# Optimization experiments

Hardware: AMD Instinct MI355X
Metric: run time of the kernel (lower is better)

## Reference

```python
import jax, jax.numpy as jnp
import numpy as np

B, S, D = 2, 2048, 2048
NH, NKV, HD = 32, 8, 64
ROPE_BASE = 10000.0


def rope(x):
    # x: [b, s, h, d]; torchtune-style interleaved-pair RoPE
    b, s, h, d = x.shape
    pos = jnp.arange(s, dtype=jnp.float32)
    inv_freq = 1.0 / (ROPE_BASE ** (jnp.arange(0, d, 2, dtype=jnp.float32) / d))
    ang = pos[:, None] * inv_freq[None, :]            # [s, d//2]
    cos = jnp.cos(ang)[None, :, None, :].astype(x.dtype)
    sin = jnp.sin(ang)[None, :, None, :].astype(x.dtype)
    xr = x.reshape(b, s, h, d // 2, 2)
    x0, x1 = xr[..., 0], xr[..., 1]
    out = jnp.stack([x0 * cos - x1 * sin, x0 * sin + x1 * cos], axis=-1)
    return out.reshape(b, s, h, d)


def setup_inputs() -> dict:
    key = jax.random.key(0)
    ks = jax.random.split(key, 5)
    return {
        "x": jax.random.normal(ks[0], (B, S, D), dtype=jnp.float32),
        "Wq": jax.random.normal(ks[1], (NH * HD, D), dtype=jnp.float32) * 0.02,
        "Wk": jax.random.normal(ks[2], (NKV * HD, D), dtype=jnp.float32) * 0.02,
        "Wv": jax.random.normal(ks[3], (NKV * HD, D), dtype=jnp.float32) * 0.02,
        "Wo": jax.random.normal(ks[4], (D, NH * HD), dtype=jnp.float32) * 0.02,
    }


def reference(x, Wq, Wk, Wv, Wo):
    b, s, _ = x.shape
    qpk = NH // NKV  # queries per kv head
    # projections (Linear, no bias)
    q = (x @ Wq.T).reshape(b, s, NH, HD)
    k = (x @ Wk.T).reshape(b, s, NKV, HD)
    v = (x @ Wv.T).reshape(b, s, NKV, HD)
    # RoPE on q and k (expanding k before RoPE == RoPE on kv heads then group-broadcast)
    q = rope(q)
    k = rope(k)
    # grouped attention: q -> [b, s, g, n, d], k/v stay [b, s, g, d]
    qg = q.reshape(b, s, NKV, qpk, HD)
    scale = 1.0 / jnp.sqrt(jnp.array(HD, dtype=x.dtype))
    scores = jnp.einsum("bqgnd,bkgd->bgnqk", qg, k) * scale  # [b,g,n,s,s]
    attn = jax.nn.softmax(scores, axis=-1)
    out = jnp.einsum("bgnqk,bkgd->bqgnd", attn, v)           # [b,s,g,n,d]
    out = out.reshape(b, s, NH * HD)
    return out @ Wo.T
```

## Files before the change

### kernel.cpp

```cpp
#include <hip/hip_runtime.h>
#include <hip/hip_bf16.h>
#include <math.h>

#define SLEN 2048
#define DMODEL 2048
#define NH 32
#define NKV 8
#define HD 64
#define BATCH 2
#define MROWS (BATCH * SLEN)
#define QKVN (NH * HD + 2 * NKV * HD)

typedef __attribute__((ext_vector_type(8))) short bf16x8;
typedef __attribute__((ext_vector_type(4))) float f32x4;
typedef __attribute__((ext_vector_type(16))) float f32x16;
typedef __attribute__((ext_vector_type(4))) unsigned u32x4;

__device__ __forceinline__ unsigned short f2bf(float f) {
  union { float f; unsigned u; } v; v.f = f;
  return (unsigned short)((v.u + 0x7FFFu + ((v.u >> 16) & 1u)) >> 16);
}
__device__ __forceinline__ float bf2f(unsigned short h) {
  union { unsigned u; float f; } v; v.u = ((unsigned)h) << 16;
  return v.f;
}
__device__ __forceinline__ unsigned cvt_pk_bf16(float lo, float hi) {
  unsigned r;
  asm("v_cvt_pk_bf16_f32 %0, %1, %2" : "=v"(r) : "v"(lo), "v"(hi));
  return r;
}
__device__ __forceinline__ float fast_exp2(float x) {
#if __has_builtin(__builtin_amdgcn_exp2f)
  return __builtin_amdgcn_exp2f(x);
#else
  return exp2f(x);
#endif
}
__device__ __forceinline__ void gload_lds16(const unsigned short* g, unsigned short* l) {
  __builtin_amdgcn_global_load_lds(
      (const __attribute__((address_space(1))) unsigned int*)(g),
      (__attribute__((address_space(3))) unsigned int*)(l), 16, 0, 0);
}

__global__ __launch_bounds__(256) void cvt_kernel(const float* __restrict__ src,
                                                  unsigned short* __restrict__ dst,
                                                  int n8) {
  const int i = blockIdx.x * 256 + threadIdx.x;
  if (i >= n8) return;
  const float4 a = *(const float4*)&src[(size_t)i * 8];
  const float4 b = *(const float4*)&src[(size_t)i * 8 + 4];
  uint4 o;
  o.x = cvt_pk_bf16(a.x, a.y);
  o.y = cvt_pk_bf16(a.z, a.w);
  o.z = cvt_pk_bf16(b.x, b.y);
  o.w = cvt_pk_bf16(b.z, b.w);
  *(uint4*)&dst[(size_t)i * 8] = o;
}

__global__ __launch_bounds__(256) void cvt_w4_kernel(
    const float* __restrict__ Wq, const float* __restrict__ Wk,
    const float* __restrict__ Wv, const float* __restrict__ Wo,
    unsigned short* __restrict__ wqkvb, unsigned short* __restrict__ wob) {
  const int i = blockIdx.x * 256 + threadIdx.x;
  const float* src;
  unsigned short* dst;
  size_t off;
  if (i < 524288)       { src = Wq; dst = wqkvb;           off = i; }
  else if (i < 655360)  { src = Wk; dst = wqkvb + 4194304; off = i - 524288; }
  else if (i < 786432)  { src = Wv; dst = wqkvb + 5242880; off = i - 655360; }
  else                  { src = Wo; dst = wob;             off = i - 786432; }
  const float4 a = *(const float4*)&src[off * 8];
  const float4 b = *(const float4*)&src[off * 8 + 4];
  uint4 o;
  o.x = cvt_pk_bf16(a.x, a.y);
  o.y = cvt_pk_bf16(a.z, a.w);
  o.z = cvt_pk_bf16(b.x, b.y);
  o.w = cvt_pk_bf16(b.z, b.w);
  *(uint4*)&dst[off * 8] = o;
}

template <int OUTBF16>
__global__ __launch_bounds__(256) void gemm_bf16_kernel(
    const unsigned short* __restrict__ A, const unsigned short* __restrict__ B,
    void* __restrict__ Cv, int M, int N, int K) {
  __shared__ unsigned short As[128][32];
  __shared__ unsigned short Bs[128][32];

  const int tid = threadIdx.x;
  const int lane = tid & 63;
  const int wid = tid >> 6;
  const int g = lane >> 4;
  const int fr = lane & 15;
  const int m0 = blockIdx.x * 128;
  const int n0 = blockIdx.y * 128;
  const int wm = (wid >> 1) * 64;
  const int wn = (wid & 1) * 64;

  const int srow = wid * 32 + (lane >> 2);
  const int scol = (lane & 3) * 8;
  const unsigned short* ga = &A[(size_t)(m0 + srow) * K + scol];
  const unsigned short* gb = &B[(size_t)(n0 + srow) * K + scol];
  unsigned short* la0 = &As[wid * 32][0];
  unsigned short* la1 = &As[wid * 32 + 16][0];
  unsigned short* lb0 = &Bs[wid * 32][0];
  unsigned short* lb1 = &Bs[wid * 32 + 16][0];
  const size_t rstep = (size_t)16 * K;

  f32x4 acc[4][4];
#pragma unroll
  for (int i = 0; i < 4; i++)
#pragma unroll
    for (int j = 0; j < 4; j++) acc[i][j] = (f32x4){0.f, 0.f, 0.f, 0.f};

  for (int kt = 0; kt < K; kt += 32) {
    __syncthreads();
    gload_lds16(ga + kt, la0);
    gload_lds16(ga + kt + rstep, la1);
    gload_lds16(gb + kt, lb0);
    gload_lds16(gb + kt + rstep, lb1);
    __syncthreads();

    bf16x8 af[4], bfr[4];
#pragma unroll
    for (int i = 0; i < 4; i++) {
      af[i] = *(const bf16x8*)&As[wm + i * 16 + fr][g * 8];
      bfr[i] = *(const bf16x8*)&Bs[wn + i * 16 + fr][g * 8];
    }
#pragma unroll
    for (int i = 0; i < 4; i++)
#pragma unroll
      for (int j = 0; j < 4; j++)
        acc[i][j] = __builtin_amdgcn_mfma_f32_16x16x32_bf16(af[i], bfr[j], acc[i][j], 0, 0, 0);
  }

  if constexpr (OUTBF16) {
    unsigned short* C = (unsigned short*)Cv;
#pragma unroll
    for (int i = 0; i < 4; i++)
#pragma unroll
      for (int j = 0; j < 4; j++)
#pragma unroll
        for (int r = 0; r < 4; r++)
          C[(size_t)(m0 + wm + i * 16 + g * 4 + r) * N + n0 + wn + j * 16 + fr] =
              f2bf(acc[i][j][r]);
  } else {
    float* C = (float*)Cv;
#pragma unroll
    for (int i = 0; i < 4; i++)
#pragma unroll
      for (int j = 0; j < 4; j++)
#pragma unroll
        for (int r = 0; r < 4; r++)
          C[(size_t)(m0 + wm + i * 16 + g * 4 + r) * N + n0 + wn + j * 16 + fr] =
              acc[i][j][r];
  }
}

__global__ __launch_bounds__(256) void rope_q_kernel(const unsigned short* __restrict__ qkvb,
                                                     unsigned short* __restrict__ qb) {
  const int idx = blockIdx.x * 256 + threadIdx.x;
  const int j = idx & 31;
  const int s = (idx >> 5) & (SLEN - 1);
  const int h = (idx >> 16) & (NH - 1);
  const int b = idx >> 21;
  const unsigned pin = *(const unsigned*)&qkvb[(size_t)(b * SLEN + s) * QKVN + h * HD + 2 * j];
  const float x0 = bf2f((unsigned short)(pin & 0xffffu));
  const float x1 = bf2f((unsigned short)(pin >> 16));
  const float inv = expf(-0.14391156831f * (float)(2 * j));
  const float ang = (float)s * inv;
  float sn, cs;
  sincosf(ang, &sn, &cs);
  const float SC = 0.18033688011f;
  const float o0 = (x0 * cs - x1 * sn) * SC;
  const float o1 = (x0 * sn + x1 * cs) * SC;
  *(unsigned*)&qb[((size_t)(b * NH + h) * SLEN + s) * HD + 2 * j] = cvt_pk_bf16(o0, o1);
}

__global__ __launch_bounds__(256) void rope_k_kernel(const unsigned short* __restrict__ qkvb,
                                                     unsigned short* __restrict__ kb) {
  const int idx = blockIdx.x * 256 + threadIdx.x;
  const int j = idx & 31;
  const int s = (idx >> 5) & (SLEN - 1);
  const int kh = (idx >> 16) & (NKV - 1);
  const int b = idx >> 19;
  const unsigned pin =
      *(const unsigned*)&qkvb[(size_t)(b * SLEN + s) * QKVN + NH * HD + kh * HD + 2 * j];
  const float x0 = bf2f((unsigned short)(pin & 0xffffu));
  const float x1 = bf2f((unsigned short)(pin >> 16));
  const float inv = expf(-0.14391156831f * (float)(2 * j));
  const float ang = (float)s * inv;
  float sn, cs;
  sincosf(ang, &sn, &cs);
  const float o0 = x0 * cs - x1 * sn;
  const float o1 = x0 * sn + x1 * cs;
  *(unsigned*)&kb[((size_t)(b * NKV + kh) * SLEN + s) * HD + 2 * j] = cvt_pk_bf16(o0, o1);
}

__global__ __launch_bounds__(256) void vcast_kernel(const unsigned short* __restrict__ qkvb,
                                                    unsigned short* __restrict__ vt) {
  __shared__ unsigned short tile[64][72];
  const int tid = threadIdx.x;
  const int bi = blockIdx.x;
  const int st = bi & 31;
  const int kh = (bi >> 5) & 7;
  const int b = bi >> 8;
  const int r = tid >> 2;
  const int c0 = (tid & 3) * 16;
  const unsigned short* src =
      &qkvb[(size_t)(b * SLEN + st * 64 + r) * QKVN + (NH + NKV) * HD + kh * HD + c0];
  *(bf16x8*)&tile[r][c0] = *(const bf16x8*)src;
  *(bf16x8*)&tile[r][c0 + 8] = *(const bf16x8*)(src + 8);
  __syncthreads();
  alignas(16) unsigned short tmp[16];
#pragma unroll
  for (int i = 0; i < 16; ++i) tmp[i] = tile[c0 + i][r];
  unsigned short* dst = &vt[((size_t)(b * NKV + kh) * HD + r) * SLEN + st * 64 + c0];
  *(bf16x8*)dst = *(bf16x8*)tmp;
  *(bf16x8*)(dst + 8) = *(bf16x8*)(tmp + 8);
}

__global__ __launch_bounds__(512) void attn_kernel(
    const unsigned short* __restrict__ qb, const unsigned short* __restrict__ kb,
    const unsigned short* __restrict__ vt, unsigned short* __restrict__ aob) {
  __shared__ unsigned short Kbuf[2][4096];
  __shared__ unsigned short Vbuf[2][4096];

  const int tid = threadIdx.x;
  const int lane = tid & 63;
  const int wid = tid >> 6;
  const int lq = lane & 31;
  const int hi = lane >> 5;
  const int sw = lane & 7;

  const int jb = blockIdx.x;
  const int xcd = jb & 7;
  const int idx = jb >> 3;
  const int bh = xcd * 8 + (idx & 7);
  const int qt = idx >> 3;
  const int b = bh >> 5, h = bh & 31;
  const int kh = h >> 2;
  const size_t qbase = (size_t)bh * SLEN * HD;
  const size_t kbase = (size_t)(b * NKV + kh) * SLEN * HD;
  const size_t vbase = (size_t)(b * NKV + kh) * HD * SLEN;

  const int q0 = qt * 256 + wid * 32;
  bf16x8 qf[4];
#pragma unroll
  for (int ks = 0; ks < 4; ++ks)
    qf[ks] = *(const bf16x8*)&qb[qbase + (size_t)(q0 + lq) * HD + ks * 16 + hi * 8];

  const int swzc = ((lane & 7) ^ ((lane >> 3) & 7)) * 8;
  const int srow = wid * 8 + (lane >> 3);
  const unsigned short* gk0 = kb + kbase + (size_t)srow * HD + swzc;
  const unsigned short* gv0 = vt + vbase + (size_t)srow * SLEN + swzc;

  f32x16 acc0 = {}, acc1 = {};
  float m = -1e30f, l = 0.f;

  gload_lds16(gk0, &Kbuf[0][wid * 512]);
  gload_lds16(gv0, &Vbuf[0][wid * 512]);

  for (int kt = 0; kt < SLEN / 64; ++kt) {
    const int cur = kt & 1;
    asm volatile("s_waitcnt vmcnt(0)" ::: "memory");
    __syncthreads();
    if (kt + 1 < SLEN / 64) {
      const int nxt = cur ^ 1;
      const size_t ko = (size_t)(kt + 1) * 64 * HD;
      const size_t vo = (size_t)(kt + 1) * 64;
      gload_lds16(gk0 + ko, &Kbuf[nxt][wid * 512]);
      gload_lds16(gv0 + vo, &Vbuf[nxt][wid * 512]);
    }

    f32x16 s0 = {}, s1 = {};
#pragma unroll
    for (int ks = 0; ks < 4; ++ks) {
      const bf16x8 kf = *(const bf16x8*)&Kbuf[cur][lq * HD + (((ks * 2 + hi) ^ sw) * 8)];
      s0 = __builtin_amdgcn_mfma_f32_32x32x16_bf16(kf, qf[ks], s0, 0, 0, 0);
    }
#pragma unroll
    for (int ks = 0; ks < 4; ++ks) {
      const bf16x8 kf = *(const bf16x8*)&Kbuf[cur][(32 + lq) * HD + (((ks * 2 + hi) ^ sw) * 8)];
      s1 = __builtin_amdgcn_mfma_f32_32x32x16_bf16(kf, qf[ks], s1, 0, 0, 0);
    }

    float tm = s0[0];
#pragma unroll
    for (int i = 1; i < 16; ++i) tm = fmaxf(tm, s0[i]);
#pragma unroll
    for (int i = 0; i < 16; ++i) tm = fmaxf(tm, s1[i]);
    tm = fmaxf(tm, __shfl_xor(tm, 32));

    if (__any(tm > m + 8.0f)) {
      const float mn = fmaxf(m, tm);
      const float corr = fast_exp2(m - mn);
      l *= corr;
#pragma unroll
      for (int i = 0; i < 16; ++i) { acc0[i] *= corr; acc1[i] *= corr; }
      m = mn;
    }

    float p0[16], p1[16];
    float lsum = 0.f;
#pragma unroll
    for (int i = 0; i < 16; ++i) { p0[i] = fast_exp2(s0[i] - m); lsum += p0[i]; }
#pragma unroll
    for (int i = 0; i < 16; ++i) { p1[i] = fast_exp2(s1[i] - m); lsum += p1[i]; }
    lsum += __shfl_xor(lsum, 32);
    l += lsum;

    unsigned u0[8], u1[8];
#pragma unroll
    for (int c = 0; c < 4; ++c) {
      u0[2 * c] = cvt_pk_bf16(p0[4 * c], p0[4 * c + 1]);
      u0[2 * c + 1] = cvt_pk_bf16(p0[4 * c + 2], p0[4 * c + 3]);
      u1[2 * c] = cvt_pk_bf16(p1[4 * c], p1[4 * c + 1]);
      u1[2 * c + 1] = cvt_pk_bf16(p1[4 * c + 2], p1[4 * c + 3]);
    }
    bf16x8 pf[4];
    {
      unsigned a0 = u0[0], b0 = u0[2];
      asm volatile("v_permlane32_swap_b32 %0, %1" : "+v"(a0), "+v"(b0));
      unsigned a1 = u0[1], b1 = u0[3];
      asm volatile("v_permlane32_swap_b32 %0, %1" : "+v"(a1), "+v"(b1));
      u32x4 t = {a0, a1, b0, b1};
      pf[0] = __builtin_bit_cast(bf16x8, t);
      unsigned a2 = u0[4], b2 = u0[6];
      asm volatile("v_permlane32_swap_b32 %0, %1" : "+v"(a2), "+v"(b2));
      unsigned a3 = u0[5], b3 = u0[7];
      asm volatile("v_permlane32_swap_b32 %0, %1" : "+v"(a3), "+v"(b3));
      u32x4 t2 = {a2, a3, b2, b3};
      pf[1] = __builtin_bit_cast(bf16x8, t2);
      unsigned a4 = u1[0], b4 = u1[2];
      asm volatile("v_permlane32_swap_b32 %0, %1" : "+v"(a4), "+v"(b4));
      unsigned a5 = u1[1], b5 = u1[3];
      asm volatile("v_permlane32_swap_b32 %0, %1" : "+v"(a5), "+v"(b5));
      u32x4 t3 = {a4, a5, b4, b5};
      pf[2] = __builtin_bit_cast(bf16x8, t3);
      unsigned a6 = u1[4], b6 = u1[6];
      asm volatile("v_permlane32_swap_b32 %0, %1" : "+v"(a6), "+v"(b6));
      unsigned a7 = u1[5], b7 = u1[7];
      asm volatile("v_permlane32_swap_b32 %0, %1" : "+v"(a7), "+v"(b7));
      u32x4 t4 = {a6, a7, b6, b7};
      pf[3] = __builtin_bit_cast(bf16x8, t4);
    }

#pragma unroll
    for (int ks = 0; ks < 4; ++ks) {
      const bf16x8 vf = *(const bf16x8*)&Vbuf[cur][lq * 64 + (((ks * 2 + hi) ^ sw) * 8)];
      acc0 = __builtin_amdgcn_mfma_f32_32x32x16_bf16(vf, pf[ks], acc0, 0, 0, 0);
    }
#pragma unroll
    for (int ks = 0; ks < 4; ++ks) {
      const bf16x8 vf = *(const bf16x8*)&Vbuf[cur][(32 + lq) * 64 + (((ks * 2 + hi) ^ sw) * 8)];
      acc1 = __builtin_amdgcn_mfma_f32_32x32x16_bf16(vf, pf[ks], acc1, 0, 0, 0);
    }
  }

  const float rl = 1.0f / l;
  const size_t obase = (size_t)(b * SLEN + q0 + lq) * DMODEL + h * HD;
#pragma unroll
  for (int c = 0; c < 4; ++c) {
    uint2 o;
    o.x = cvt_pk_bf16(acc0[4 * c] * rl, acc0[4 * c + 1] * rl);
    o.y = cvt_pk_bf16(acc0[4 * c + 2] * rl, acc0[4 * c + 3] * rl);
    *(uint2*)&aob[obase + 8 * c + 4 * hi] = o;
    uint2 o2;
    o2.x = cvt_pk_bf16(acc1[4 * c] * rl, acc1[4 * c + 1] * rl);
    o2.y = cvt_pk_bf16(acc1[4 * c + 2] * rl, acc1[4 * c + 3] * rl);
    *(uint2*)&aob[obase + 32 + 8 * c + 4 * hi] = o2;
  }
}

extern "C" void kernel_launch(void* const* d_in, const int* in_sizes, int n_in,
                              void* d_out, int out_size, void* d_ws, size_t ws_size,
                              hipStream_t stream) {
  const float* x  = (const float*)d_in[0];
  const float* Wq = (const float*)d_in[1];
  const float* Wk = (const float*)d_in[2];
  const float* Wv = (const float*)d_in[3];
  const float* Wo = (const float*)d_in[4];
  float* out = (float*)d_out;

  char* ws = (char*)d_ws;
  unsigned short* qkvb = (unsigned short*)ws; ws += (size_t)MROWS * QKVN * 2;
  unsigned short* qb = (unsigned short*)ws;   ws += (size_t)BATCH * NH * SLEN * HD * 2;
  unsigned short* kb = (unsigned short*)ws;   ws += (size_t)BATCH * NKV * SLEN * HD * 2;
  unsigned short* vt = (unsigned short*)ws;   ws += (size_t)BATCH * NKV * HD * SLEN * 2;
  unsigned short* xb = (unsigned short*)ws;   ws += (size_t)MROWS * DMODEL * 2;
  unsigned short* aob = xb;
  unsigned short* wqkvb = (unsigned short*)ws; ws += (size_t)QKVN * DMODEL * 2;
  unsigned short* wob = (unsigned short*)ws;

  dim3 blk(256);

  cvt_kernel<<<(MROWS * DMODEL / 8 + 255) / 256, blk, 0, stream>>>(x, xb, MROWS * DMODEL / 8);
  cvt_w4_kernel<<<(1310720 + 255) / 256, blk, 0, stream>>>(Wq, Wk, Wv, Wo, wqkvb, wob);

  gemm_bf16_kernel<1><<<dim3(MROWS / 128, QKVN / 128), blk, 0, stream>>>(
      xb, wqkvb, qkvb, MROWS, QKVN, DMODEL);

  rope_q_kernel<<<(BATCH * NH * SLEN * 32) / 256, blk, 0, stream>>>(qkvb, qb);
  rope_k_kernel<<<(BATCH * NKV * SLEN * 32) / 256, blk, 0, stream>>>(qkvb, kb);
  vcast_kernel<<<BATCH * NKV * (SLEN / 64), blk, 0, stream>>>(qkvb, vt);

  attn_kernel<<<dim3(512), dim3(512), 0, stream>>>(qb, kb, vt, aob);

  gemm_bf16_kernel<0><<<dim3(MROWS / 128, DMODEL / 128), blk, 0, stream>>>(
      aob, wob, out, MROWS, DMODEL, DMODEL);
}
```

Measured before the change: 243.8 us.

## Fuse Q RoPE into attention, merge conversion and K/V prep kernels

Q RoPE and scaling now run inside the attention kernel, which reads raw Q straight from the QKV projection output, so the separate Q buffer and its write/read pass go away. The x and weight conversion kernels are merged into one launch, and K RoPE and the V transpose share a single kernel. The cross-half row reductions in softmax use v_permlane32_swap instead of shfl_xor. This removes launches and a full Q round trip through memory, at the cost of extra sincos/exp work in the attention prologue.

```diff
diff --git a/kernel.cpp b/kernel.cpp
--- a/kernel.cpp
+++ b/kernel.cpp
@@ -36,39 +36,39 @@
   return exp2f(x);
 #endif
 }
+__device__ __forceinline__ float red32_max(float x) {
+  float a = x, b;
+  asm volatile("v_mov_b32 %0, %1" : "=v"(b) : "v"(x));
+  asm volatile("v_permlane32_swap_b32 %0, %1" : "+v"(a), "+v"(b));
+  return fmaxf(a, b);
+}
+__device__ __forceinline__ float red32_add(float x) {
+  float a = x, b;
+  asm volatile("v_mov_b32 %0, %1" : "=v"(b) : "v"(x));
+  asm volatile("v_permlane32_swap_b32 %0, %1" : "+v"(a), "+v"(b));
+  return a + b;
+}
 __device__ __forceinline__ void gload_lds16(const unsigned short* g, unsigned short* l) {
   __builtin_amdgcn_global_load_lds(
       (const __attribute__((address_space(1))) unsigned int*)(g),
       (__attribute__((address_space(3))) unsigned int*)(l), 16, 0, 0);
 }
 
-__global__ __launch_bounds__(256) void cvt_kernel(const float* __restrict__ src,
-                                                  unsigned short* __restrict__ dst,
-                                                  int n8) {
-  const int i = blockIdx.x * 256 + threadIdx.x;
-  if (i >= n8) return;
-  const float4 a = *(const float4*)&src[(size_t)i * 8];
-  const float4 b = *(const float4*)&src[(size_t)i * 8 + 4];
-  uint4 o;
-  o.x = cvt_pk_bf16(a.x, a.y);
-  o.y = cvt_pk_bf16(a.z, a.w);
-  o.z = cvt_pk_bf16(b.x, b.y);
-  o.w = cvt_pk_bf16(b.z, b.w);
-  *(uint4*)&dst[(size_t)i * 8] = o;
-}
-
-__global__ __launch_bounds__(256) void cvt_w4_kernel(
+__global__ __launch_bounds__(256) void cvt_all_kernel(
+    const float* __restrict__ x,
     const float* __restrict__ Wq, const float* __restrict__ Wk,
     const float* __restrict__ Wv, const float* __restrict__ Wo,
-    unsigned short* __restrict__ wqkvb, unsigned short* __restrict__ wob) {
+    unsigned short* __restrict__ xb, unsigned short* __restrict__ wqkvb,
+    unsigned short* __restrict__ wob) {
   const int i = blockIdx.x * 256 + threadIdx.x;
   const float* src;
   unsigned short* dst;
   size_t off;
-  if (i < 524288)       { src = Wq; dst = wqkvb;           off = i; }
-  else if (i < 655360)  { src = Wk; dst = wqkvb + 4194304; off = i - 524288; }
-  else if (i < 786432)  { src = Wv; dst = wqkvb + 5242880; off = i - 655360; }
-  else                  { src = Wo; dst = wob;             off = i - 786432; }
+  if (i < 1048576)      { src = x;  dst = xb;              off = i; }
+  else if (i < 1572864) { src = Wq; dst = wqkvb;           off = i - 1048576; }
+  else if (i < 1703936) { src = Wk; dst = wqkvb + 4194304; off = i - 1572864; }
+  else if (i < 1835008) { src = Wv; dst = wqkvb + 5242880; off = i - 1703936; }
+  else                  { src = Wo; dst = wob;             off = i - 1835008; }
   const float4 a = *(const float4*)&src[off * 8];
   const float4 b = *(const float4*)&src[off * 8 + 4];
   uint4 o;
@@ -156,71 +156,52 @@
   }
 }
 
-__global__ __launch_bounds__(256) void rope_q_kernel(const unsigned short* __restrict__ qkvb,
-                                                     unsigned short* __restrict__ qb) {
-  const int idx = blockIdx.x * 256 + threadIdx.x;
-  const int j = idx & 31;
-  const int s = (idx >> 5) & (SLEN - 1);
-  const int h = (idx >> 16) & (NH - 1);
-  const int b = idx >> 21;
-  const unsigned pin = *(const unsigned*)&qkvb[(size_t)(b * SLEN + s) * QKVN + h * HD + 2 * j];
-  const float x0 = bf2f((unsigned short)(pin & 0xffffu));
-  const float x1 = bf2f((unsigned short)(pin >> 16));
-  const float inv = expf(-0.14391156831f * (float)(2 * j));
-  const float ang = (float)s * inv;
-  float sn, cs;
-  sincosf(ang, &sn, &cs);
-  const float SC = 0.18033688011f;
-  const float o0 = (x0 * cs - x1 * sn) * SC;
-  const float o1 = (x0 * sn + x1 * cs) * SC;
-  *(unsigned*)&qb[((size_t)(b * NH + h) * SLEN + s) * HD + 2 * j] = cvt_pk_bf16(o0, o1);
-}
-
-__global__ __launch_bounds__(256) void rope_k_kernel(const unsigned short* __restrict__ qkvb,
-                                                     unsigned short* __restrict__ kb) {
-  const int idx = blockIdx.x * 256 + threadIdx.x;
-  const int j = idx & 31;
-  const int s = (idx >> 5) & (SLEN - 1);
-  const int kh = (idx >> 16) & (NKV - 1);
-  const int b = idx >> 19;
-  const unsigned pin =
-      *(const unsigned*)&qkvb[(size_t)(b * SLEN + s) * QKVN + NH * HD + kh * HD + 2 * j];
-  const float x0 = bf2f((unsigned short)(pin & 0xffffu));
-  const float x1 = bf2f((unsigned short)(pin >> 16));
-  const float inv = expf(-0.14391156831f * (float)(2 * j));
-  const float ang = (float)s * inv;
-  float sn, cs;
-  sincosf(ang, &sn, &cs);
-  const float o0 = x0 * cs - x1 * sn;
-  const float o1 = x0 * sn + x1 * cs;
-  *(unsigned*)&kb[((size_t)(b * NKV + kh) * SLEN + s) * HD + 2 * j] = cvt_pk_bf16(o0, o1);
-}
-
-__global__ __launch_bounds__(256) void vcast_kernel(const unsigned short* __restrict__ qkvb,
-                                                    unsigned short* __restrict__ vt) {
+__global__ __launch_bounds__(256) void kv_prep_kernel(const unsigned short* __restrict__ qkvb,
+                                                      unsigned short* __restrict__ kb,
+                                                      unsigned short* __restrict__ vt) {
   __shared__ unsigned short tile[64][72];
+  const int bi = blockIdx.x;
   const int tid = threadIdx.x;
-  const int bi = blockIdx.x;
-  const int st = bi & 31;
-  const int kh = (bi >> 5) & 7;
-  const int b = bi >> 8;
-  const int r = tid >> 2;
-  const int c0 = (tid & 3) * 16;
-  const unsigned short* src =
-      &qkvb[(size_t)(b * SLEN + st * 64 + r) * QKVN + (NH + NKV) * HD + kh * HD + c0];
-  *(bf16x8*)&tile[r][c0] = *(const bf16x8*)src;
-  *(bf16x8*)&tile[r][c0 + 8] = *(const bf16x8*)(src + 8);
-  __syncthreads();
-  alignas(16) unsigned short tmp[16];
-#pragma unroll
-  for (int i = 0; i < 16; ++i) tmp[i] = tile[c0 + i][r];
-  unsigned short* dst = &vt[((size_t)(b * NKV + kh) * HD + r) * SLEN + st * 64 + c0];
-  *(bf16x8*)dst = *(bf16x8*)tmp;
-  *(bf16x8*)(dst + 8) = *(bf16x8*)(tmp + 8);
+  if (bi < 4096) {
+    const int idx = bi * 256 + tid;
+    const int j = idx & 31;
+    const int s = (idx >> 5) & (SLEN - 1);
+    const int kh = (idx >> 16) & (NKV - 1);
+    const int b = idx >> 19;
+    const unsigned pin =
+        *(const unsigned*)&qkvb[(size_t)(b * SLEN + s) * QKVN + NH * HD + kh * HD + 2 * j];
+    const float x0 = bf2f((unsigned short)(pin & 0xffffu));
+    const float x1 = bf2f((unsigned short)(pin >> 16));
+    const float inv = expf(-0.14391156831f * (float)(2 * j));
+    const float ang = (float)s * inv;
+    float sn, cs;
+    sincosf(ang, &sn, &cs);
+    const float o0 = x0 * cs - x1 * sn;
+    const float o1 = x0 * sn + x1 * cs;
+    *(unsigned*)&kb[((size_t)(b * NKV + kh) * SLEN + s) * HD + 2 * j] = cvt_pk_bf16(o0, o1);
+  } else {
+    const int bv = bi - 4096;
+    const int st = bv & 31;
+    const int kh = (bv >> 5) & 7;
+    const int b = bv >> 8;
+    const int r = tid >> 2;
+    const int c0 = (tid & 3) * 16;
+    const unsigned short* src =
+        &qkvb[(size_t)(b * SLEN + st * 64 + r) * QKVN + (NH + NKV) * HD + kh * HD + c0];
+    *(bf16x8*)&tile[r][c0] = *(const bf16x8*)src;
+    *(bf16x8*)&tile[r][c0 + 8] = *(const bf16x8*)(src + 8);
+    __syncthreads();
+    alignas(16) unsigned short tmp[16];
+#pragma unroll
+    for (int i = 0; i < 16; ++i) tmp[i] = tile[c0 + i][r];
+    unsigned short* dst = &vt[((size_t)(b * NKV + kh) * HD + r) * SLEN + st * 64 + c0];
+    *(bf16x8*)dst = *(bf16x8*)tmp;
+    *(bf16x8*)(dst + 8) = *(bf16x8*)(tmp + 8);
+  }
 }
 
 __global__ __launch_bounds__(512) void attn_kernel(
-    const unsigned short* __restrict__ qb, const unsigned short* __restrict__ kb,
+    const unsigned short* __restrict__ qkvb, const unsigned short* __restrict__ kb,
     const unsigned short* __restrict__ vt, unsigned short* __restrict__ aob) {
   __shared__ unsigned short Kbuf[2][4096];
   __shared__ unsigned short Vbuf[2][4096];
@@ -239,15 +220,31 @@
   const int qt = idx >> 3;
   const int b = bh >> 5, h = bh & 31;
   const int kh = h >> 2;
-  const size_t qbase = (size_t)bh * SLEN * HD;
   const size_t kbase = (size_t)(b * NKV + kh) * SLEN * HD;
   const size_t vbase = (size_t)(b * NKV + kh) * HD * SLEN;
 
   const int q0 = qt * 256 + wid * 32;
+  const int s = q0 + lq;
+  const unsigned short* qsrc = &qkvb[(size_t)(b * SLEN + s) * QKVN + h * HD];
   bf16x8 qf[4];
 #pragma unroll
-  for (int ks = 0; ks < 4; ++ks)
-    qf[ks] = *(const bf16x8*)&qb[qbase + (size_t)(q0 + lq) * HD + ks * 16 + hi * 8];
+  for (int ks = 0; ks < 4; ++ks) {
+    const bf16x8 raw = *(const bf16x8*)(qsrc + ks * 16 + hi * 8);
+    unsigned pk[4];
+#pragma unroll
+    for (int p = 0; p < 4; ++p) {
+      const int j = ks * 8 + hi * 4 + p;
+      const float inv = expf(-0.14391156831f * (float)(2 * j));
+      float sn, cs;
+      sincosf((float)s * inv, &sn, &cs);
+      const float SC = 0.18033688011f;
+      const float x0 = bf2f((unsigned short)raw[2 * p]);
+      const float x1 = bf2f((unsigned short)raw[2 * p + 1]);
+      pk[p] = cvt_pk_bf16((x0 * cs - x1 * sn) * SC, (x0 * sn + x1 * cs) * SC);
+    }
+    u32x4 t = {pk[0], pk[1], pk[2], pk[3]};
+    qf[ks] = __builtin_bit_cast(bf16x8, t);
+  }
 
   const int swzc = ((lane & 7) ^ ((lane >> 3) & 7)) * 8;
   const int srow = wid * 8 + (lane >> 3);
@@ -289,7 +286,7 @@
     for (int i = 1; i < 16; ++i) tm = fmaxf(tm, s0[i]);
 #pragma unroll
     for (int i = 0; i < 16; ++i) tm = fmaxf(tm, s1[i]);
-    tm = fmaxf(tm, __shfl_xor(tm, 32));
+    tm = red32_max(tm);
 
     if (__any(tm > m + 8.0f)) {
       const float mn = fmaxf(m, tm);
@@ -306,8 +303,7 @@
     for (int i = 0; i < 16; ++i) { p0[i] = fast_exp2(s0[i] - m); lsum += p0[i]; }
 #pragma unroll
     for (int i = 0; i < 16; ++i) { p1[i] = fast_exp2(s1[i] - m); lsum += p1[i]; }
-    lsum += __shfl_xor(lsum, 32);
-    l += lsum;
+    l += red32_add(lsum);
 
     unsigned u0[8], u1[8];
 #pragma unroll
@@ -384,7 +380,6 @@
 
   char* ws = (char*)d_ws;
   unsigned short* qkvb = (unsigned short*)ws; ws += (size_t)MROWS * QKVN * 2;
-  unsigned short* qb = (unsigned short*)ws;   ws += (size_t)BATCH * NH * SLEN * HD * 2;
   unsigned short* kb = (unsigned short*)ws;   ws += (size_t)BATCH * NKV * SLEN * HD * 2;
   unsigned short* vt = (unsigned short*)ws;   ws += (size_t)BATCH * NKV * HD * SLEN * 2;
   unsigned short* xb = (unsigned short*)ws;   ws += (size_t)MROWS * DMODEL * 2;
@@ -394,17 +389,14 @@
 
   dim3 blk(256);
 
-  cvt_kernel<<<(MROWS * DMODEL / 8 + 255) / 256, blk, 0, stream>>>(x, xb, MROWS * DMODEL / 8);
-  cvt_w4_kernel<<<(1310720 + 255) / 256, blk, 0, stream>>>(Wq, Wk, Wv, Wo, wqkvb, wob);
+  cvt_all_kernel<<<9216, blk, 0, stream>>>(x, Wq, Wk, Wv, Wo, xb, wqkvb, wob);
 
   gemm_bf16_kernel<1><<<dim3(MROWS / 128, QKVN / 128), blk, 0, stream>>>(
       xb, wqkvb, qkvb, MROWS, QKVN, DMODEL);
 
-  rope_q_kernel<<<(BATCH * NH * SLEN * 32) / 256, blk, 0, stream>>>(qkvb, qb);
-  rope_k_kernel<<<(BATCH * NKV * SLEN * 32) / 256, blk, 0, stream>>>(qkvb, kb);
-  vcast_kernel<<<BATCH * NKV * (SLEN / 64), blk, 0, stream>>>(qkvb, vt);
-
-  attn_kernel<<<dim3(512), dim3(512), 0, stream>>>(qb, kb, vt, aob);
+  kv_prep_kernel<<<4608, blk, 0, stream>>>(qkvb, kb, vt);
+
+  attn_kernel<<<dim3(512), dim3(512), 0, stream>>>(qkvb, kb, vt, aob);
 
   gemm_bf16_kernel<0><<<dim3(MROWS / 128, DMODEL / 128), blk, 0, stream>>>(
       aob, wob, out, MROWS, DMODEL, DMODEL);
```

Measured after the change: 234.1 us. 1.04x faster.
